# Optimization experiments

Hardware: AMD Instinct MI355X
Metric: run time of the kernel (lower is better)

## Reference

```python
import jax, jax.numpy as jnp
import numpy as np

NUM_HEADS = 8
EPS = 1e-12  # torch F.normalize default eps


def _l2norm(t):
    # t / max(||t||_2, eps) along last axis (matches F.normalize)
    n = jnp.sqrt(jnp.sum(t * t, axis=-1, keepdims=True))
    return t / jnp.maximum(n, EPS)


def setup_inputs() -> dict:
    key = jax.random.key(0)
    k1, k2, k3 = jax.random.split(key, 3)
    B, N, C = 8, 1024, 768
    x = jax.random.normal(k1, (B, N, C), dtype=jnp.float32)
    w_qkv = jax.random.normal(k2, (C, 3 * C), dtype=jnp.float32) * 0.02
    temperature = jnp.ones((NUM_HEADS, 1, 1), dtype=jnp.float32)
    w_proj = jax.random.normal(k3, (C, C), dtype=jnp.float32) * 0.02
    b_proj = jnp.zeros((C,), dtype=jnp.float32)
    return {"x": x, "w_qkv": w_qkv, "temperature": temperature,
            "w_proj": w_proj, "b_proj": b_proj}


def reference(x, w_qkv, temperature, w_proj, b_proj):
    B, N, C = x.shape
    H = NUM_HEADS
    hd = C // H
    # qkv projection (no bias), split into q,k,v of shape [B,H,N,hd]
    qkv = (x @ w_qkv).reshape(B, N, 3, H, hd)
    qkv = jnp.transpose(qkv, (2, 0, 3, 1, 4))  # [3,B,H,N,hd]
    q, k, v = qkv[0], qkv[1], qkv[2]
    q = _l2norm(q)
    k = _l2norm(k)
    # NOTE: code (unlike canonical XCA) does NOT transpose q/k, so attn is [B,H,N,N]
    attn = jnp.einsum('bhnd,bhmd->bhnm', q, k) * temperature  # temp broadcasts over B
    attn = jax.nn.softmax(attn, axis=-1)
    out = jnp.einsum('bhnm,bhmd->bhnd', attn, v)  # [B,H,N,hd]
    out = jnp.transpose(out, (0, 2, 1, 3)).reshape(B, N, C)
    return out @ w_proj + b_proj
```

## Files before the change

### kernel.cpp

```cpp
#include <hip/hip_runtime.h>
#include <math.h>

typedef __attribute__((ext_vector_type(8))) short bf16x8;
typedef __attribute__((ext_vector_type(4))) float f32x4;
typedef __attribute__((ext_vector_type(4))) unsigned int u32x4;
typedef unsigned short u16;
typedef unsigned int u32;


__device__ __forceinline__ u16 f2b(float f) {
  u32 u = __float_as_uint(f);
  return (u16)((u + 0x7fffu + ((u >> 16) & 1u)) >> 16);
}
__device__ __forceinline__ float b2f(u16 h) {
  return __uint_as_float(((u32)h) << 16);
}
__device__ __forceinline__ int swz(int m) { return (m ^ (m >> 2)) & 3; }

__device__ __forceinline__ void async16(const void* g, void* l) {
  __builtin_amdgcn_global_load_lds((const __attribute__((address_space(1))) u32*)g,
                                   (__attribute__((address_space(3))) u32*)l, 16, 0, 0);
}

template<int N> __device__ __forceinline__ void wait_vmcnt();
template<> __device__ __forceinline__ void wait_vmcnt<0>() {
  asm volatile("s_waitcnt vmcnt(0)" ::: "memory");
}
template<> __device__ __forceinline__ void wait_vmcnt<3>() {
  asm volatile("s_waitcnt vmcnt(3)" ::: "memory");
}
template<> __device__ __forceinline__ void wait_vmcnt<5>() {
  asm volatile("s_waitcnt vmcnt(5)" ::: "memory");
}

__global__ __launch_bounds__(256) void prep_kernel(const float* __restrict__ x,
                                                   const float* __restrict__ w_qkv,
                                                   const float* __restrict__ w_proj,
                                                   u16* __restrict__ xb,
                                                   u16* __restrict__ wqkvT,
                                                   u16* __restrict__ wprojT) {
  __shared__ float t[32][33];
  const int blk = blockIdx.x;
  if (blk < 6144) {
    const int idx = blk * 256 + threadIdx.x;
    const float4 v = ((const float4*)x)[idx];
    uint2 o;
    o.x = (u32)f2b(v.x) | ((u32)f2b(v.y) << 16);
    o.y = (u32)f2b(v.z) | ((u32)f2b(v.w) << 16);
    ((uint2*)xb)[idx] = o;
    return;
  }
  const float* in; u16* out; int R, C, bx, by;
  if (blk < 6144 + 1728) {
    const int rem = blk - 6144;
    in = w_qkv; out = wqkvT; R = 768; C = 2304; bx = rem % 72; by = rem / 72;
  } else {
    const int rem = blk - 6144 - 1728;
    in = w_proj; out = wprojT; R = 768; C = 768; bx = rem % 24; by = rem / 24;
  }
  const int c0 = bx * 32, r0 = by * 32;
  const int tc = threadIdx.x & 31, tr = threadIdx.x >> 5;
#pragma unroll
  for (int j = 0; j < 4; ++j)
    t[tr + j * 8][tc] = in[(size_t)(r0 + tr + j * 8) * C + c0 + tc];
  __syncthreads();
#pragma unroll
  for (int j = 0; j < 4; ++j)
    out[(size_t)(c0 + tr + j * 8) * R + r0 + tc] = f2b(t[tc][tr + j * 8]);
}

template<int NT>
__device__ __forceinline__ void gemm_core(const u16* __restrict__ A,
                                          const u16* __restrict__ Bt,
                                          int m0, int n0, f32x4 acc[4][NT / 32]) {
  constexpr int JT = NT / 32;
  constexpr int NG = 512 + NT * 4;
  constexpr int NINST = NG / 256;
  __shared__ u16 Sm[3 * NG * 8];
  const int tid = threadIdx.x;
  const int w = tid >> 6, lane = tid & 63;
  const int i15 = lane & 15, quad = lane >> 4;
  const int wm = (w >> 1) * 64, wn = (w & 1) * (NT / 2);
  const int sw = quad ^ swz(i15);

#pragma unroll
  for (int i = 0; i < 4; ++i)
#pragma unroll
    for (int j = 0; j < JT; ++j) acc[i][j] = (f32x4){0.f, 0.f, 0.f, 0.f};

  const u16* gsrc[NINST];
#pragma unroll
  for (int inst = 0; inst < NINST; ++inst) {
    const int s = inst * 256 + tid;
    if (s < 512) {
      const int m = s >> 2, e = s & 3;
      gsrc[inst] = A + ((size_t)(m0 + m) * 768 + (e ^ swz(m)) * 8);
    } else {
      const int s2 = s - 512;
      const int n = s2 >> 2, e = s2 & 3;
      gsrc[inst] = Bt + ((size_t)(n0 + n) * 768 + (e ^ swz(n)) * 8);
    }
  }

  auto stage = [&](int bsel) {
#pragma unroll
    for (int inst = 0; inst < NINST; ++inst) {
      async16(gsrc[inst], (void*)(Sm + ((size_t)bsel * NG + inst * 256 + w * 64) * 8));
      gsrc[inst] += 32;
    }
  };

  stage(0);
  stage(1);

  for (int t = 0; t < 24; ++t) {
    if (t < 23) wait_vmcnt<NINST>();
    else        wait_vmcnt<0>();
    __builtin_amdgcn_s_barrier();
    __builtin_amdgcn_sched_barrier(0);
    if (t < 22) stage((t + 2) % 3);
    const u16* buf = Sm + (size_t)(t % 3) * NG * 8;
    bf16x8 af[4], bf[JT];
#pragma unroll
    for (int i = 0; i < 4; ++i)
      af[i] = *(const bf16x8*)(buf + ((size_t)(wm + i * 16 + i15) * 4 + sw) * 8);
#pragma unroll
    for (int j = 0; j < JT; ++j)
      bf[j] = *(const bf16x8*)(buf + ((size_t)512 + (wn + j * 16 + i15) * 4 + sw) * 8);
#pragma unroll
    for (int i = 0; i < 4; ++i)
#pragma unroll
      for (int j = 0; j < JT; ++j)
        acc[i][j] = __builtin_amdgcn_mfma_f32_16x16x32_bf16(af[i], bf[j], acc[i][j], 0, 0, 0);
  }
}

__global__ __launch_bounds__(256, 2) void qkv_gemm_kernel(
    const u16* __restrict__ xb, const u16* __restrict__ wT,
    const float* __restrict__ temp,
    u16* __restrict__ q, u16* __restrict__ k, u16* __restrict__ vT) {
  f32x4 acc[4][6];
  const int bid = blockIdx.x;
  const int xcd = bid & 7, slot = bid >> 3;
  const int mb = xcd * 8 + slot / 12, nb = slot % 12;
  const int m0 = mb * 128, n0 = nb * 192;
  gemm_core<192>(xb, wT, m0, n0, acc);

  const int tid = threadIdx.x, w = tid >> 6, lane = tid & 63;
  const int i15 = lane & 15, quad = lane >> 4;
  const int wm = (w >> 1) * 64;
  const int three = nb >> 2;
  const int h = ((nb & 3) << 1) + (w & 1);

  if (three < 2) {
    u16* dst = three ? k : q;
    const float sc_extra = three ? 1.f : temp[h];
#pragma unroll
    for (int it = 0; it < 4; ++it) {
#pragma unroll
      for (int r = 0; r < 4; ++r) {
        float s = 0.f;
#pragma unroll
        for (int jt = 0; jt < 6; ++jt) s += acc[it][jt][r] * acc[it][jt][r];
        s += __shfl_xor(s, 1); s += __shfl_xor(s, 2);
        s += __shfl_xor(s, 4); s += __shfl_xor(s, 8);
        const float scale = sc_extra / fmaxf(sqrtf(s), 1e-12f);
        const int m = m0 + wm + it * 16 + quad * 4 + r;
        const int b = m >> 10, n = m & 1023;
        u16* rowp = dst + ((size_t)(b * 8 + h) * 1024 + n) * 96;
#pragma unroll
        for (int jt = 0; jt < 6; ++jt)
          rowp[jt * 16 + i15] = f2b(acc[it][jt][r] * scale);
      }
    }
  } else {
#pragma unroll
    for (int it = 0; it < 4; ++it) {
      const int mb4 = m0 + wm + it * 16 + quad * 4;
      const int b = mb4 >> 10, nbase = mb4 & 1023;
#pragma unroll
      for (int jt = 0; jt < 6; ++jt) {
        const int d = jt * 16 + i15;
        uint2 pk;
        pk.x = (u32)f2b(acc[it][jt][0]) | ((u32)f2b(acc[it][jt][1]) << 16);
        pk.y = (u32)f2b(acc[it][jt][2]) | ((u32)f2b(acc[it][jt][3]) << 16);
        *(uint2*)(vT + ((size_t)(b * 8 + h) * 96 + d) * 1024 + nbase) = pk;
      }
    }
  }
}

__global__ __launch_bounds__(512, 4) void attn_kernel(
    const u16* __restrict__ q, const u16* __restrict__ kk,
    const u16* __restrict__ vT, u16* __restrict__ ctx) {
  __shared__ u16 smem[32768];
  const int tid = threadIdx.x, w = tid >> 6, lane = tid & 63;
  const int i15 = lane & 15, quad = lane >> 4;
  const int xs = swz(i15);
  const int bh = blockIdx.x & 63, qbase = (blockIdx.x >> 6) * 128;
  const int b = bh >> 3, h = bh & 7;
  u16* Pw = smem + 24576 + w * 1024;

  bf16x8 qf[3];
  {
    const int qrow = qbase + w * 16 + i15;
    const u16* qp = q + ((size_t)bh * 1024 + qrow) * 96 + quad * 8;
#pragma unroll
    for (int c = 0; c < 3; ++c) qf[c] = *(const bf16x8*)(qp + c * 32);
  }

  const u16* gsrc[3]; int gstep[3];
#pragma unroll
  for (int inst = 0; inst < 3; ++inst) {
    const int s = inst * 512 + tid;
    if (s < 768) {
      const int key6 = (s & 255) >> 2, c = s >> 8;
      const int e = c * 4 + ((s & 3) ^ swz(key6));
      gsrc[inst] = kk + ((size_t)bh * 1024 + key6) * 96 + e * 8;
      gstep[inst] = 64 * 96;
    } else {
      const int s2 = s - 768, r = s2 >> 2;
      const int c2 = (r >= 96), d = r - 96 * c2;
      gsrc[inst] = vT + ((size_t)bh * 96 + d) * 1024 + c2 * 32 + ((s2 & 3) ^ swz(d)) * 8;
      gstep[inst] = 64;
    }
  }

#pragma unroll
  for (int inst = 0; inst < 3; ++inst)
    async16(gsrc[inst], (void*)(smem + (size_t)(inst * 512 + w * 64) * 8));

  f32x4 o[6];
#pragma unroll
  for (int dt = 0; dt < 6; ++dt) o[dt] = (f32x4){0.f, 0.f, 0.f, 0.f};
  float l = 0.f;

  for (int t = 0; t < 16; ++t) {
    __syncthreads();
    const u16* KVs = smem + (t & 1) * 12288;
    if (t < 15) {
      u16* dst = smem + ((t + 1) & 1) * 12288;
#pragma unroll
      for (int inst = 0; inst < 3; ++inst) {
        gsrc[inst] += gstep[inst];
        async16(gsrc[inst], (void*)(dst + (size_t)(inst * 512 + w * 64) * 8));
      }
    }
#pragma unroll
    for (int kt = 0; kt < 4; ++kt) {
      bf16x8 af[3];
#pragma unroll
      for (int c = 0; c < 3; ++c)
        af[c] = *(const bf16x8*)(KVs + ((size_t)((c * 64 + kt * 16 + i15) * 4) + (quad ^ xs)) * 8);
      f32x4 s = (f32x4){0.f, 0.f, 0.f, 0.f};
#pragma unroll
      for (int c = 0; c < 3; ++c)
        s = __builtin_amdgcn_mfma_f32_16x16x32_bf16(af[c], qf[c], s, 0, 0, 0);
      const float e0 = __expf(s[0]), e1 = __expf(s[1]);
      const float e2 = __expf(s[2]), e3 = __expf(s[3]);
      l += (e0 + e1) + (e2 + e3);
      uint2 pk;
      pk.x = (u32)f2b(e0) | ((u32)f2b(e1) << 16);
      pk.y = (u32)f2b(e2) | ((u32)f2b(e3) << 16);
      const int pg = (kt & 1) * 2 + (quad >> 1);
      *(uint2*)(Pw + (size_t)(((kt >> 1) * 16 + i15) * 4 + (pg ^ xs)) * 8
                    + (quad & 1) * 4) = pk;
    }
#pragma unroll
    for (int c2 = 0; c2 < 2; ++c2) {
      const bf16x8 pa = *(const bf16x8*)(Pw + (size_t)((c2 * 16 + i15) * 4 + (quad ^ xs)) * 8);
#pragma unroll
      for (int dt = 0; dt < 6; ++dt) {
        const bf16x8 vb = *(const bf16x8*)(KVs +
            ((size_t)(768 + (c2 * 96 + dt * 16 + i15) * 4) + (quad ^ xs)) * 8);
        o[dt] = __builtin_amdgcn_mfma_f32_16x16x32_bf16(pa, vb, o[dt], 0, 0, 0);
      }
    }
  }

  l += __shfl_xor(l, 16); l += __shfl_xor(l, 32);
  __syncthreads();
  u16* scr = smem + w * 1664;
#pragma unroll
  for (int r = 0; r < 4; ++r) {
    const float linv = 1.f / __shfl(l, quad * 4 + r);
    const int row16 = quad * 4 + r;
#pragma unroll
    for (int dt = 0; dt < 6; ++dt)
      scr[row16 * 104 + dt * 16 + i15] = f2b(o[dt][r] * linv);
  }
#pragma unroll
  for (int jj = 0; jj < 3; ++jj) {
    const int id = jj * 64 + lane;
    const int row16 = id / 12, g = id - row16 * 12;
    const int grow = b * 1024 + qbase + w * 16 + row16;
    *(uint4*)(ctx + (size_t)grow * 768 + h * 96 + g * 8) =
        *(const uint4*)(scr + row16 * 104 + g * 8);
  }
}

__global__ __launch_bounds__(256, 4) void proj_gemm_kernel(
    const u16* __restrict__ ctx, const u16* __restrict__ wT,
    const float* __restrict__ bias, float* __restrict__ out) {
  f32x4 acc[4][2];
  const int bid = blockIdx.x;
  const int xcd = bid & 7, slot = bid >> 3;
  const int mb = xcd * 8 + slot / 12, nb = slot % 12;
  const int m0 = mb * 128, n0 = nb * 64;
  gemm_core<64>(ctx, wT, m0, n0, acc);

  const int tid = threadIdx.x, w = tid >> 6, lane = tid & 63;
  const int i15 = lane & 15, quad = lane >> 4;
  const int wm = (w >> 1) * 64, wn = (w & 1) * 32;
#pragma unroll
  for (int jt = 0; jt < 2; ++jt) {
    const int c = n0 + wn + jt * 16 + i15;
    const float bb = bias[c];
#pragma unroll
    for (int it = 0; it < 4; ++it) {
#pragma unroll
      for (int r = 0; r < 4; ++r) {
        const int m = m0 + wm + it * 16 + quad * 4 + r;
        out[(size_t)m * 768 + c] = acc[it][jt][r] + bb;
      }
    }
  }
}

extern "C" void kernel_launch(void* const* d_in, const int* in_sizes, int n_in,
                              void* d_out, int out_size, void* d_ws, size_t ws_size,
                              hipStream_t stream) {
  const float* x      = (const float*)d_in[0];
  const float* w_qkv  = (const float*)d_in[1];
  const float* temp   = (const float*)d_in[2];
  const float* w_proj = (const float*)d_in[3];
  const float* b_proj = (const float*)d_in[4];

  u16* ws      = (u16*)d_ws;
  u16* xb      = ws;
  u16* wqkvT   = xb + 6291456;
  u16* qb      = wqkvT + 1769472;
  u16* kb      = qb + 6291456;
  u16* vTb     = kb + 6291456;
  u16* ctxb    = vTb + 6291456;
  u16* wprojT  = ctxb + 6291456;

  prep_kernel<<<8448, 256, 0, stream>>>(x, w_qkv, w_proj, xb, wqkvT, wprojT);
  qkv_gemm_kernel<<<768, 256, 0, stream>>>(xb, wqkvT, temp, qb, kb, vTb);
  attn_kernel<<<512, 512, 0, stream>>>(qb, kb, vTb, ctxb);
  proj_gemm_kernel<<<768, 256, 0, stream>>>(ctxb, wprojT, b_proj, (float*)d_out);
}
```

Before: 180.6 us.

## Software-pipeline attention S and PV phases and simplify QKV GEMM staging

The attention loop is restructured so the QK^T/exp phase for tile t+1 runs while the PV MMAs for tile t execute. K gets triple buffering and V double buffering in a larger LDS allocation, and the launch-bounds occupancy hint drops from 4 to 2. The QKV GEMM switches to a single-buffer synchronous staging loop with higher occupancy (3 blocks), trading load/compute overlap within a block for more resident blocks. The larger LDS footprint and the extra barriers per k-step may limit latency hiding.

```diff
diff --git a/kernel.cpp b/kernel.cpp
--- a/kernel.cpp
+++ b/kernel.cpp
@@ -28,9 +28,6 @@
 }
 template<> __device__ __forceinline__ void wait_vmcnt<3>() {
   asm volatile("s_waitcnt vmcnt(3)" ::: "memory");
-}
-template<> __device__ __forceinline__ void wait_vmcnt<5>() {
-  asm volatile("s_waitcnt vmcnt(5)" ::: "memory");
 }
 
 __global__ __launch_bounds__(256) void prep_kernel(const float* __restrict__ x,
@@ -70,9 +67,59 @@
 }
 
 template<int NT>
-__device__ __forceinline__ void gemm_core(const u16* __restrict__ A,
-                                          const u16* __restrict__ Bt,
-                                          int m0, int n0, f32x4 acc[4][NT / 32]) {
+__device__ __forceinline__ void gemm_core2b(const u16* __restrict__ A,
+                                            const u16* __restrict__ Bt,
+                                            int m0, int n0, f32x4 acc[4][NT / 32]) {
+  constexpr int JT = NT / 32;
+  constexpr int NINST = (512 + NT * 4) / 256;
+  __shared__ u16 Sm[(512 + NT * 4) * 8];
+  const int tid = threadIdx.x;
+  const int w = tid >> 6, lane = tid & 63;
+  const int i15 = lane & 15, quad = lane >> 4;
+  const int wm = (w >> 1) * 64, wn = (w & 1) * (NT / 2);
+  const int sw = quad ^ swz(i15);
+
+#pragma unroll
+  for (int i = 0; i < 4; ++i)
+#pragma unroll
+    for (int j = 0; j < JT; ++j) acc[i][j] = (f32x4){0.f, 0.f, 0.f, 0.f};
+
+  for (int k0 = 0; k0 < 768; k0 += 32) {
+    __syncthreads();
+#pragma unroll
+    for (int inst = 0; inst < NINST; ++inst) {
+      const int s = inst * 256 + tid;
+      const u16* src;
+      if (inst < 2) {
+        const int m = s >> 2, e = s & 3;
+        src = A + ((size_t)(m0 + m) * 768 + k0 + (e ^ swz(m)) * 8);
+      } else {
+        const int s2 = s - 512;
+        const int n = s2 >> 2, e = s2 & 3;
+        src = Bt + ((size_t)(n0 + n) * 768 + k0 + (e ^ swz(n)) * 8);
+      }
+      async16(src, (void*)(Sm + (size_t)(inst * 256 + w * 64) * 8));
+    }
+    __syncthreads();
+    bf16x8 af[4], bf[JT];
+#pragma unroll
+    for (int i = 0; i < 4; ++i)
+      af[i] = *(const bf16x8*)(Sm + ((size_t)(wm + i * 16 + i15) * 4 + sw) * 8);
+#pragma unroll
+    for (int j = 0; j < JT; ++j)
+      bf[j] = *(const bf16x8*)(Sm + ((size_t)512 + (wn + j * 16 + i15) * 4 + sw) * 8);
+#pragma unroll
+    for (int i = 0; i < 4; ++i)
+#pragma unroll
+      for (int j = 0; j < JT; ++j)
+        acc[i][j] = __builtin_amdgcn_mfma_f32_16x16x32_bf16(af[i], bf[j], acc[i][j], 0, 0, 0);
+  }
+}
+
+template<int NT>
+__device__ __forceinline__ void gemm_core_c3(const u16* __restrict__ A,
+                                             const u16* __restrict__ Bt,
+                                             int m0, int n0, f32x4 acc[4][NT / 32]) {
   constexpr int JT = NT / 32;
   constexpr int NG = 512 + NT * 4;
   constexpr int NINST = NG / 256;
@@ -135,7 +182,7 @@
   }
 }
 
-__global__ __launch_bounds__(256, 2) void qkv_gemm_kernel(
+__global__ __launch_bounds__(256, 3) void qkv_gemm_kernel(
     const u16* __restrict__ xb, const u16* __restrict__ wT,
     const float* __restrict__ temp,
     u16* __restrict__ q, u16* __restrict__ k, u16* __restrict__ vT) {
@@ -144,7 +191,7 @@
   const int xcd = bid & 7, slot = bid >> 3;
   const int mb = xcd * 8 + slot / 12, nb = slot % 12;
   const int m0 = mb * 128, n0 = nb * 192;
-  gemm_core<192>(xb, wT, m0, n0, acc);
+  gemm_core2b<192>(xb, wT, m0, n0, acc);
 
   const int tid = threadIdx.x, w = tid >> 6, lane = tid & 63;
   const int i15 = lane & 15, quad = lane >> 4;
@@ -190,16 +237,16 @@
   }
 }
 
-__global__ __launch_bounds__(512, 4) void attn_kernel(
+__global__ __launch_bounds__(512, 2) void attn_kernel(
     const u16* __restrict__ q, const u16* __restrict__ kk,
     const u16* __restrict__ vT, u16* __restrict__ ctx) {
-  __shared__ u16 smem[32768];
+  __shared__ u16 smem[38912];
   const int tid = threadIdx.x, w = tid >> 6, lane = tid & 63;
   const int i15 = lane & 15, quad = lane >> 4;
   const int xs = swz(i15);
   const int bh = blockIdx.x & 63, qbase = (blockIdx.x >> 6) * 128;
   const int b = bh >> 3, h = bh & 7;
-  u16* Pw = smem + 24576 + w * 1024;
+  u16* Pw = smem + 30720 + w * 1024;
 
   bf16x8 qf[3];
   {
@@ -209,49 +256,42 @@
     for (int c = 0; c < 3; ++c) qf[c] = *(const bf16x8*)(qp + c * 32);
   }
 
-  const u16* gsrc[3]; int gstep[3];
-#pragma unroll
-  for (int inst = 0; inst < 3; ++inst) {
-    const int s = inst * 512 + tid;
-    if (s < 768) {
-      const int key6 = (s & 255) >> 2, c = s >> 8;
-      const int e = c * 4 + ((s & 3) ^ swz(key6));
-      gsrc[inst] = kk + ((size_t)bh * 1024 + key6) * 96 + e * 8;
-      gstep[inst] = 64 * 96;
-    } else {
-      const int s2 = s - 768, r = s2 >> 2;
-      const int c2 = (r >= 96), d = r - 96 * c2;
-      gsrc[inst] = vT + ((size_t)bh * 96 + d) * 1024 + c2 * 32 + ((s2 & 3) ^ swz(d)) * 8;
-      gstep[inst] = 64;
-    }
-  }
-
-#pragma unroll
-  for (int inst = 0; inst < 3; ++inst)
-    async16(gsrc[inst], (void*)(smem + (size_t)(inst * 512 + w * 64) * 8));
+  const u16 *kb0, *kb1, *vb0, *vb1;
+  {
+    int s = tid, key = (s & 255) >> 2, c = s >> 8;
+    kb0 = kk + ((size_t)bh * 1024 + key) * 96 + (c * 4 + ((s & 3) ^ swz(key))) * 8;
+    s = 512 + tid; key = (s & 255) >> 2; c = s >> 8;
+    kb1 = kk + ((size_t)bh * 1024 + key) * 96 + (c * 4 + ((s & 3) ^ swz(key))) * 8;
+    int s2 = tid, r = s2 >> 2, c2 = (r >= 96), d = r - 96 * c2;
+    vb0 = vT + ((size_t)bh * 96 + d) * 1024 + c2 * 32 + ((s2 & 3) ^ swz(d)) * 8;
+    s2 = 512 + tid; r = s2 >> 2; c2 = (r >= 96); d = r - 96 * c2;
+    vb1 = vT + ((size_t)bh * 96 + d) * 1024 + c2 * 32 + ((s2 & 3) ^ swz(d)) * 8;
+  }
+  auto stageK = [&](int tt, int kbuf) {
+    u16* dst = smem + kbuf * 6144;
+    async16(kb0 + (size_t)tt * 64 * 96, (void*)(dst + (size_t)(w * 64) * 8));
+    if (tid < 256)
+      async16(kb1 + (size_t)tt * 64 * 96, (void*)(dst + (size_t)(512 + w * 64) * 8));
+  };
+  auto stageV = [&](int tt, int vbuf) {
+    u16* dst = smem + 18432 + vbuf * 6144;
+    async16(vb0 + tt * 64, (void*)(dst + (size_t)(w * 64) * 8));
+    if (tid < 256)
+      async16(vb1 + tt * 64, (void*)(dst + (size_t)(512 + w * 64) * 8));
+  };
 
   f32x4 o[6];
 #pragma unroll
   for (int dt = 0; dt < 6; ++dt) o[dt] = (f32x4){0.f, 0.f, 0.f, 0.f};
   float l = 0.f;
 
-  for (int t = 0; t < 16; ++t) {
-    __syncthreads();
-    const u16* KVs = smem + (t & 1) * 12288;
-    if (t < 15) {
-      u16* dst = smem + ((t + 1) & 1) * 12288;
-#pragma unroll
-      for (int inst = 0; inst < 3; ++inst) {
-        gsrc[inst] += gstep[inst];
-        async16(gsrc[inst], (void*)(dst + (size_t)(inst * 512 + w * 64) * 8));
-      }
-    }
+  auto S_phase = [&](const u16* Kb) {
 #pragma unroll
     for (int kt = 0; kt < 4; ++kt) {
       bf16x8 af[3];
 #pragma unroll
       for (int c = 0; c < 3; ++c)
-        af[c] = *(const bf16x8*)(KVs + ((size_t)((c * 64 + kt * 16 + i15) * 4) + (quad ^ xs)) * 8);
+        af[c] = *(const bf16x8*)(Kb + ((size_t)((c * 64 + kt * 16 + i15) * 4) + (quad ^ xs)) * 8);
       f32x4 s = (f32x4){0.f, 0.f, 0.f, 0.f};
 #pragma unroll
       for (int c = 0; c < 3; ++c)
@@ -266,15 +306,30 @@
       *(uint2*)(Pw + (size_t)(((kt >> 1) * 16 + i15) * 4 + (pg ^ xs)) * 8
                     + (quad & 1) * 4) = pk;
     }
-#pragma unroll
-    for (int c2 = 0; c2 < 2; ++c2) {
-      const bf16x8 pa = *(const bf16x8*)(Pw + (size_t)((c2 * 16 + i15) * 4 + (quad ^ xs)) * 8);
-#pragma unroll
-      for (int dt = 0; dt < 6; ++dt) {
-        const bf16x8 vb = *(const bf16x8*)(KVs +
-            ((size_t)(768 + (c2 * 96 + dt * 16 + i15) * 4) + (quad ^ xs)) * 8);
-        o[dt] = __builtin_amdgcn_mfma_f32_16x16x32_bf16(pa, vb, o[dt], 0, 0, 0);
-      }
+  };
+
+  stageK(0, 0); stageV(0, 0);
+  __syncthreads();
+  stageK(1, 1); stageV(1, 1);
+  S_phase(smem);
+
+  for (int t = 0; t < 16; ++t) {
+    const bf16x8 pa0 = *(const bf16x8*)(Pw + (size_t)((i15 * 4) + (quad ^ xs)) * 8);
+    const bf16x8 pa1 = *(const bf16x8*)(Pw + (size_t)(((16 + i15) * 4) + (quad ^ xs)) * 8);
+    __syncthreads();
+    if (t < 14) stageK(t + 2, (t + 2) % 3);
+    if (t < 15) stageV(t + 1, (t + 1) & 1);
+    if (t < 15) S_phase(smem + ((t + 1) % 3) * 6144);
+    const u16* Vb = smem + 18432 + (t & 1) * 6144;
+#pragma unroll
+    for (int dt = 0; dt < 6; ++dt) {
+      const bf16x8 vb = *(const bf16x8*)(Vb + ((size_t)((dt * 16 + i15) * 4) + (quad ^ xs)) * 8);
+      o[dt] = __builtin_amdgcn_mfma_f32_16x16x32_bf16(pa0, vb, o[dt], 0, 0, 0);
+    }
+#pragma unroll
+    for (int dt = 0; dt < 6; ++dt) {
+      const bf16x8 vb = *(const bf16x8*)(Vb + ((size_t)(((96 + dt * 16 + i15) * 4)) + (quad ^ xs)) * 8);
+      o[dt] = __builtin_amdgcn_mfma_f32_16x16x32_bf16(pa1, vb, o[dt], 0, 0, 0);
     }
   }
 
@@ -307,7 +362,7 @@
   const int xcd = bid & 7, slot = bid >> 3;
   const int mb = xcd * 8 + slot / 12, nb = slot % 12;
   const int m0 = mb * 128, n0 = nb * 64;
-  gemm_core<64>(ctx, wT, m0, n0, acc);
+  gemm_core_c3<64>(ctx, wT, m0, n0, acc);
 
   const int tid = threadIdx.x, w = tid >> 6, lane = tid & 63;
   const int i15 = lane & 15, quad = lane >> 4;
```

Measured after the change: 180.7 us. About the same (+0.1%).
